# Kernel tuning notes

Hardware: AMD Instinct MI355X
Metric: run time of the kernel (lower is better)

## Reference

```python
import jax, jax.numpy as jnp
import numpy as np

NUM_BFS_ROUNDS = 32      # fixed-iteration replacement for the set-based BFS (enough hops for N=4096, k=20)
VORONOI_CHUNK = 1024     # must divide B*N


def _knn_self(points, K):
    # brute-force self-KNN over [B,N,3]; idx[...,0] is the query point itself
    sq = jnp.sum(points * points, -1)
    dist = sq[:, :, None] + sq[:, None, :] - 2.0 * jnp.einsum('bnd,bmd->bnm', points, points)
    N = points.shape[1]
    dist = jnp.where(jnp.eye(N, dtype=bool)[None], -1.0, dist)  # force self to rank first
    _, idx = jax.lax.top_k(-dist, K)
    return idx  # [B,N,K] int32


def _gather(x, idx):
    # x [B,N,D], idx [B,N,K] -> [B,N,K,D]
    return jax.vmap(lambda xb, ib: xb[ib])(x, idx)


def _disambiguate(normals, idx):
    # BFS normal-orientation propagation from point 0 (frontier shared across batch, as in the torch code)
    B, N, _ = normals.shape
    frontier0 = jnp.zeros((N,), bool).at[0].set(True)
    visited0 = jnp.zeros((N,), bool)

    def step(carry, _):
        nrm, visited, frontier = carry
        safe_idx = jnp.where(frontier[None, :, None], idx, N)  # non-frontier rows scatter to dummy slot N
        cur = _gather(nrm, idx)                                 # [B,N,K,3]
        sign = jnp.where(jnp.sum(cur * cur[:, :, 0:1, :], -1, keepdims=True) > 0, 1.0, -1.0)
        renew = cur * sign

        def scat(nb, ib, rb):
            pad = jnp.concatenate([nb, jnp.zeros((1, 3), nb.dtype)], 0)
            return pad.at[ib.reshape(-1)].set(rb.reshape(-1, 3))[:N]

        nrm = jax.vmap(scat)(nrm, safe_idx, renew)
        mark = jnp.zeros((N + 1,), bool).at[safe_idx[:, :, 1:].reshape(-1)].set(True)[:N]
        visited = visited | frontier
        frontier = mark & ~visited
        return (nrm, visited, frontier), None

    (normals, _, _), _ = jax.lax.scan(step, (normals, visited0, frontier0), None, length=NUM_BFS_ROUNDS)
    return normals


def _frames_field(points, idx):
    knn_pts = _gather(points, idx)                              # [B,N,K,3]
    centered = knn_pts - knn_pts.mean(-2, keepdims=True)
    # NOTE: divides by (last_dim - 1) == 2, faithfully replicating the original code
    cov = jnp.einsum('bnki,bnkj->bnij', centered, centered) / 2.0
    _, vecs = jnp.linalg.eigh(cov)                              # ascending eigenvalues
    frames = jnp.swapaxes(vecs, -1, -2)                         # rows = eigenvectors; row 0 = normal
    frames = frames.at[:, :, 0, :].set(_disambiguate(frames[:, :, 0, :], idx))
    det = jnp.linalg.det(frames)
    frames = frames.at[:, :, 1, :].set(frames[:, :, 1, :] * det[..., None])
    return frames, knn_pts


def _forward(points, k, local_W):
    B, N = points.shape[:2]
    idx = _knn_self(points, k)
    frames, knn_pts = _frames_field(points, idx)
    dpt = knn_pts - points[:, :, None, :]                       # [B,N,K,3]
    t1 = frames[:, :, 1, :]
    t2 = frames[:, :, 2, :]
    dpt_t = jnp.stack([jnp.sum(dpt * t1[:, :, None, :], -1),
                       jnp.sum(dpt * t2[:, :, None, :], -1)], -1)   # [B,N,K,2]

    # ---- local voronoi area on tangent-plane grid ----
    bmin = dpt_t.min(-2) * 1.1                                  # [B,N,2]
    bmax = dpt_t.max(-2) * 1.1
    maxlen = (bmax - bmin).max(-1)                              # [B,N]
    coord = (dpt_t - bmin[:, :, None, :]) / maxlen[:, :, None, None] * 2.0 - 1.0
    lin = jnp.linspace(-1.0, 1.0, local_W, dtype=points.dtype)
    X, Y = jnp.meshgrid(lin, lin, indexing='ij')
    grid = jnp.stack([X, Y], -1).reshape(-1, 2)                 # [W^2, 2]
    coords_c = jax.lax.stop_gradient(coord).reshape(-1, VORONOI_CHUNK, k, 2)

    def chunk_count(c):  # c [C,k,2] -> count of grid cells whose nearest local point is the center (idx 0)
        d = jnp.sum((grid[None, :, None, :] - c[:, None, :, :]) ** 2, -1)  # [C,W^2,k]
        return jnp.sum(jnp.argmin(d, -1) == 0, -1)

    counts = jax.lax.map(chunk_count, coords_c).reshape(B, N).astype(points.dtype)
    area = counts * maxlen ** 2 / float((local_W - 1) ** 2)     # [B,N]

    # ---- Weingarten fields (non-strict branch) -> gaussian curvature ----
    normals = frames[:, :, 0, :]
    dnrm = _gather(normals, idx) - normals[:, :, None, :]
    dnrm_t = jnp.stack([jnp.sum(dnrm * t1[:, :, None, :], -1),
                        jnp.sum(dnrm * t2[:, :, None, :], -1)], -1)  # [B,N,K,2]
    XXT = jnp.einsum('bnki,bnkj->bnij', dpt_t, dpt_t)
    YXT = jnp.einsum('bnki,bnkj->bnij', dnrm_t, dpt_t)
    Wmat = YXT @ jnp.linalg.inv(XXT + 1e-8 * jnp.eye(2, dtype=points.dtype))
    Wmat = (Wmat + jnp.swapaxes(Wmat, -1, -2)) / 2.0
    gauss = jnp.linalg.det(Wmat)                                # [B,N]

    euler = jnp.sum(gauss * area, -1) / np.pi / 2.0             # [B]
    return euler


def setup_inputs() -> dict:
    key = jax.random.key(0)
    pointscloud = jax.random.normal(key, (2, 4096, 3), dtype=jnp.float32)
    return {"pointscloud": pointscloud, "k": 20, "local_W": 64}


def reference(pointscloud, k, local_W):
    return _forward(pointscloud, k, local_W)
```

## Files before the change

### kernel.cpp

```cpp
#include <hip/hip_runtime.h>
#include <math.h>

#define NPTS  4096
#define BATCH 2
#define KNB   20
#define WGRID 64
#define GCELLS (WGRID * WGRID)
#define NROUNDS 32
#define KBUF  192
#define KQ    16
#define NEDGE (BATCH * NPTS * KNB)
#define NPACK (NEDGE / 16)

__global__ __launch_bounds__(256) void prep_kernel(const float* __restrict__ pts,
                                                   float4* __restrict__ pts4) {
    const int i = blockIdx.x * 256 + threadIdx.x;
    const float x = pts[i * 3 + 0], y = pts[i * 3 + 1], z = pts[i * 3 + 2];
    pts4[i] = make_float4(x, y, z, x * x + y * y + z * z);
}

__device__ __forceinline__ float knn_dist(const float4 c, const float px,
                                          const float py, const float pz,
                                          const float sqn, const int m,
                                          const int n) {
    const float dot = px * c.x + py * c.y + pz * c.z;
    float dist = (sqn + c.w) - 2.0f * dot;
    if (m == n) dist = -1.0f;
    return dist;
}

__device__ __forceinline__ unsigned long long knn_key(const float dist, const int m) {
    unsigned u = __float_as_uint(dist);
    u = (dist < 0.0f) ? ~u : (u | 0x80000000u);
    return ((unsigned long long)u << 32) | (unsigned)m;
}

__global__ __launch_bounds__(1024, 8) void knn_kernel(const float4* __restrict__ pts4,
                                                      int* __restrict__ idx) {
    const int tid  = threadIdx.x;
    const int lane = tid & 63;
    const int wid  = tid >> 6;
    const int q    = blockIdx.x * KQ + wid;
    const int b    = q >> 12;
    const int n    = q & (NPTS - 1);
    const float4* P4 = pts4 + (size_t)b * NPTS;

    __shared__ float4 spts[NPTS];
    __shared__ unsigned short buf[KQ][KBUF];

    for (int i = tid; i < NPTS; i += 1024) spts[i] = P4[i];
    __syncthreads();

    const float4 me = spts[n];
    const float px = me.x, py = me.y, pz = me.z, sqn = me.w;

    float lmin = 3e38f;
#pragma unroll
    for (int step = 0; step < 64; ++step) {
        const int m = lane + step * 64;
        lmin = fminf(lmin, knn_dist(spts[m], px, py, pz, sqn, m, n));
    }

    float v = lmin;
#pragma unroll
    for (int k = 2; k <= 64; k <<= 1) {
#pragma unroll
        for (int j = k >> 1; j >= 1; j >>= 1) {
            const float o = __shfl_xor(v, j, 64);
            const bool up    = ((lane & k) == 0);
            const bool lower = ((lane & j) == 0);
            v = (lower == up) ? fminf(v, o) : fmaxf(v, o);
        }
    }
    float thr = __shfl(v, 19, 64);
    thr = thr + fabsf(thr) * 1e-4f + 1e-6f;

    unsigned short* wbuf = buf[wid];
    int cnt = 0;
#pragma unroll
    for (int step = 0; step < 64; ++step) {
        const int m = lane + step * 64;
        const float dist = knn_dist(spts[m], px, py, pz, sqn, m, n);
        const bool keep = (dist <= thr);
        const unsigned long long mask = __ballot(keep);
        if (keep) {
            const int pos = cnt + __popcll(mask & ((1ull << lane) - 1ull));
            if (pos < KBUF) wbuf[pos] = (unsigned short)m;
        }
        cnt += __popcll(mask);
    }

    const int M = (cnt < KBUF) ? cnt : KBUF;
    int* op = idx + (size_t)q * KNB;
    const unsigned long long MAXK = ~0ull;
    if (M <= 64) {
        unsigned long long key = MAXK;
        if (lane < M) {
            const int m = (int)wbuf[lane];
            key = knn_key(knn_dist(spts[m], px, py, pz, sqn, m, n), m);
        }
#pragma unroll
        for (int k = 2; k <= 64; k <<= 1) {
#pragma unroll
            for (int j = k >> 1; j >= 1; j >>= 1) {
                const unsigned long long o = __shfl_xor(key, j, 64);
                const bool up    = ((lane & k) == 0);
                const bool lower = ((lane & j) == 0);
                const bool takeMin = (lower == up);
                const unsigned long long mn = key < o ? key : o;
                const unsigned long long mx = key < o ? o : key;
                key = takeMin ? mn : mx;
            }
        }
        if (lane < KNB) op[lane] = (int)(unsigned)(key & 0xffffffffu);
    } else {
        unsigned long long s0 = MAXK, s1 = MAXK, s2 = MAXK;
        if (lane < M) {
            const int m = (int)wbuf[lane];
            s0 = knn_key(knn_dist(spts[m], px, py, pz, sqn, m, n), m);
        }
        if (lane + 64 < M) {
            const int m = (int)wbuf[lane + 64];
            s1 = knn_key(knn_dist(spts[m], px, py, pz, sqn, m, n), m);
        }
        if (lane + 128 < M) {
            const int m = (int)wbuf[lane + 128];
            s2 = knn_key(knn_dist(spts[m], px, py, pz, sqn, m, n), m);
        }
#pragma unroll 1
        for (int r = 0; r < KNB; ++r) {
            unsigned long long kk = s0 < s1 ? s0 : s1;
            kk = kk < s2 ? kk : s2;
#pragma unroll
            for (int off = 32; off; off >>= 1) {
                const unsigned long long ok = __shfl_xor(kk, off, 64);
                kk = ok < kk ? ok : kk;
            }
            if (s0 == kk) s0 = MAXK;
            else if (s1 == kk) s1 = MAXK;
            else if (s2 == kk) s2 = MAXK;
            if (lane == 0) op[r] = (int)(unsigned)(kk & 0xffffffffu);
        }
    }
}

template <int p, int q, int r>
__device__ __forceinline__ void jrot(double A[3][3], double V[3][3]) {
    double apq = A[p][q];
    if (fabs(apq) < 1e-300) return;
    double app = A[p][p], aqq = A[q][q];
    double tau = (aqq - app) / (2.0 * apq);
    double sq  = sqrt(1.0 + tau * tau);
    double t   = (tau >= 0.0) ? (1.0 / (tau + sq)) : (1.0 / (tau - sq));
    double c   = 1.0 / sqrt(1.0 + t * t);
    double s   = t * c;
    A[p][p] = app - t * apq; A[q][q] = aqq + t * apq;
    A[p][q] = 0.0; A[q][p] = 0.0;
    double arp = A[r][p], arq = A[r][q];
    A[r][p] = c * arp - s * arq; A[p][r] = A[r][p];
    A[r][q] = s * arp + c * arq; A[q][r] = A[r][q];
#pragma unroll
    for (int i = 0; i < 3; ++i) {
        double vip = V[i][p], viq = V[i][q];
        V[i][p] = c * vip - s * viq;
        V[i][q] = s * vip + c * viq;
    }
}

__device__ __forceinline__ double selV(const double V[3][3], int i, int c) {
    return c == 0 ? V[i][0] : (c == 1 ? V[i][1] : V[i][2]);
}

__global__ __launch_bounds__(64) void frames_kernel(const float* __restrict__ pts,
                                                    const int* __restrict__ idx,
                                                    float* __restrict__ frames,
                                                    float* __restrict__ normals) {
    const int g = blockIdx.x * 64 + threadIdx.x;
    const int b = g / NPTS;
    const float* P  = pts + (size_t)b * NPTS * 3;
    const int*   ip = idx + (size_t)g * KNB;

    float mx = 0.f, my = 0.f, mz = 0.f;
#pragma unroll
    for (int k = 0; k < KNB; ++k) {
        const int j = ip[k];
        mx += P[j * 3 + 0]; my += P[j * 3 + 1]; mz += P[j * 3 + 2];
    }
    mx /= 20.0f; my /= 20.0f; mz /= 20.0f;

    float c00 = 0.f, c01 = 0.f, c02 = 0.f, c11 = 0.f, c12 = 0.f, c22 = 0.f;
#pragma unroll
    for (int k = 0; k < KNB; ++k) {
        const int j = ip[k];
        const float x = P[j * 3 + 0] - mx;
        const float y = P[j * 3 + 1] - my;
        const float z = P[j * 3 + 2] - mz;
        c00 += x * x; c01 += x * y; c02 += x * z;
        c11 += y * y; c12 += y * z; c22 += z * z;
    }
    c00 *= 0.5f; c01 *= 0.5f; c02 *= 0.5f; c11 *= 0.5f; c12 *= 0.5f; c22 *= 0.5f;

    double A[3][3] = {{c00, c01, c02}, {c01, c11, c12}, {c02, c12, c22}};
    double V[3][3] = {{1, 0, 0}, {0, 1, 0}, {0, 0, 1}};
#pragma unroll
    for (int sw = 0; sw < 10; ++sw) {
        jrot<0, 1, 2>(A, V);
        jrot<0, 2, 1>(A, V);
        jrot<1, 2, 0>(A, V);
    }
    double e0 = A[0][0], e1 = A[1][1], e2 = A[2][2];
    int o0 = 0, o1 = 1, o2 = 2;
    if (e0 > e1) { double t = e0; e0 = e1; e1 = t; int o = o0; o0 = o1; o1 = o; }
    if (e1 > e2) { double t = e1; e1 = e2; e2 = t; int o = o1; o1 = o2; o2 = o; }
    if (e0 > e1) { double t = e0; e0 = e1; e1 = t; int o = o0; o0 = o1; o1 = o; }

    float* F = frames + (size_t)g * 9;
    F[0] = (float)selV(V, 0, o0); F[1] = (float)selV(V, 1, o0); F[2] = (float)selV(V, 2, o0);
    F[3] = (float)selV(V, 0, o1); F[4] = (float)selV(V, 1, o1); F[5] = (float)selV(V, 2, o1);
    F[6] = (float)selV(V, 0, o2); F[7] = (float)selV(V, 1, o2); F[8] = (float)selV(V, 2, o2);
    normals[(size_t)g * 3 + 0] = F[0];
    normals[(size_t)g * 3 + 1] = F[1];
    normals[(size_t)g * 3 + 2] = F[2];
}

__global__ __launch_bounds__(256) void edgesign_kernel(const int* __restrict__ idx,
                                                       const float* __restrict__ normals,
                                                       unsigned* __restrict__ dsgnp,
                                                       unsigned short* __restrict__ idx16) {
    const int e = blockIdx.x * 256 + threadIdx.x;
    const int lane = threadIdx.x & 63;
    const int b = e / (NPTS * KNB);
    const int r = e - b * NPTS * KNB;
    const int n = r / KNB;
    const int j = idx[e];
    idx16[e] = (unsigned short)j;
    const float* NB = normals + (size_t)b * NPTS * 3;
    const float d = __fadd_rn(__fadd_rn(__fmul_rn(NB[j * 3 + 0], NB[n * 3 + 0]),
                                        __fmul_rn(NB[j * 3 + 1], NB[n * 3 + 1])),
                              __fmul_rn(NB[j * 3 + 2], NB[n * 3 + 2]));
    const unsigned long long m0 = __ballot(d == 0.0f);
    const unsigned long long m1 = __ballot(d > 0.0f);
    if (lane < 4) {
        unsigned x = (unsigned)(m0 >> (lane * 16)) & 0xFFFFu;
        unsigned y = (unsigned)(m1 >> (lane * 16)) & 0xFFFFu;
        x = (x | (x << 8)) & 0x00FF00FFu; x = (x | (x << 4)) & 0x0F0F0F0Fu;
        x = (x | (x << 2)) & 0x33333333u; x = (x | (x << 1)) & 0x55555555u;
        y = (y | (y << 8)) & 0x00FF00FFu; y = (y | (y << 4)) & 0x0F0F0F0Fu;
        y = (y | (y << 2)) & 0x33333333u; y = (y | (y << 1)) & 0x55555555u;
        dsgnp[((e - lane) >> 4) + lane] = x | (y << 1);
    }
}

__global__ __launch_bounds__(1024) void bfs_kernel(const unsigned short* __restrict__ idx16,
                                                   const unsigned* __restrict__ dsgnp,
                                                   float* __restrict__ nrm) {
    const int tid = threadIdx.x;
    const int lane = tid & 63;
    __shared__ int winner[BATCH * NPTS];
    __shared__ signed char sgbuf[2][BATCH * NPTS];
    __shared__ unsigned dsp[NPACK];
    __shared__ unsigned short list[NPTS];
    __shared__ unsigned char EL[NPTS];
    __shared__ int cntsh;

    for (int j = tid; j < NPTS; j += 1024) {
        winner[j] = 0; winner[NPTS + j] = 0;
        sgbuf[0][j] = 1; sgbuf[0][NPTS + j] = 1;
        EL[j] = 0;
    }
    for (int i = tid; i < NPACK; i += 1024) dsp[i] = dsgnp[i];
    if (tid == 0) { cntsh = 1; list[0] = 0; EL[0] = 1; }
    __syncthreads();

    int cur = 0;
    int rstart = 0, rend = 1;
    for (int round = 0; round < NROUNDS; ++round) {
        const int tag = (round + 1) << 17;
        const int items = (rend - rstart) * BATCH;
        for (int base = 0; base < items; base += 4096) {
            unsigned pr[4][KNB / 2];
            int tflat[4], wbase[4];
            bool ok[4];
#pragma unroll
            for (int s = 0; s < 4; ++s) {
                const int w = base + s * 1024 + tid;
                ok[s] = (w < items);
                if (ok[s]) {
                    const int i = w >> 1, b = w & 1;
                    const int n0 = (int)list[rstart + i];
                    tflat[s] = tag + n0 * KNB;
                    wbase[s] = b * NPTS;
                    const unsigned* rp =
                        (const unsigned*)(idx16 + ((size_t)b * NPTS + n0) * KNB);
#pragma unroll
                    for (int u = 0; u < KNB / 2; ++u) pr[s][u] = rp[u];
                }
            }
#pragma unroll
            for (int s = 0; s < 4; ++s) {
                if (ok[s]) {
#pragma unroll
                    for (int u = 0; u < KNB / 2; ++u) {
                        const int j0 = (int)(pr[s][u] & 0xffffu);
                        const int j1 = (int)(pr[s][u] >> 16);
                        atomicMax(&winner[wbase[s] + j0], tflat[s] + 2 * u);
                        atomicMax(&winner[wbase[s] + j1], tflat[s] + 2 * u + 1);
                    }
                }
            }
        }
        __syncthreads();
        const signed char* sgOld = sgbuf[cur];
        signed char* sgNew = sgbuf[cur ^ 1];
#pragma unroll
        for (int u = 0; u < 4; ++u) {
            const int j = tid + u * 1024;
            bool marked = false;
#pragma unroll
            for (int b = 0; b < BATCH; ++b) {
                const int bj = b * NPTS + j;
                const int w = winner[bj];
                signed char s = sgOld[bj];
                if (w >= tag) {
                    const int flat = w - tag;
                    const int nsrc = flat / KNB;
                    const int wi = b * (NPTS * KNB) + flat;
                    const int d = (int)((dsp[wi >> 4] >> ((wi & 15) << 1)) & 3u) - 1;
                    const signed char sn = sgOld[b * NPTS + nsrc];
                    s = d ? (signed char)(d * sn) : (signed char)(-s);
                    if (flat % KNB != 0) marked = true;
                }
                sgNew[bj] = s;
            }
            const bool f = marked && !EL[j];
            if (f) EL[j] = 1;
            const unsigned long long mask = __ballot(f);
            if (mask) {
                const int lead = (int)(__ffsll((long long)mask) - 1);
                int basep = 0;
                if (lane == lead) basep = atomicAdd(&cntsh, (int)__popcll(mask));
                basep = __shfl(basep, lead, 64);
                if (f) list[basep + (int)__popcll(mask & ((1ull << lane) - 1ull))] =
                           (unsigned short)j;
            }
        }
        __syncthreads();
        cur ^= 1;
        rstart = rend;
        rend = cntsh;
        if (rstart == rend) break;
    }
    const signed char* sgF = sgbuf[cur];
    for (int i = tid; i < BATCH * NPTS * 3; i += 1024) {
        if (sgF[i / 3] < 0) nrm[i] = -nrm[i];
    }
}

__global__ __launch_bounds__(256) void geom_kernel(const float* __restrict__ pts,
                                                   const int* __restrict__ idx,
                                                   const float* __restrict__ frames,
                                                   const float* __restrict__ nrm,
                                                   double* __restrict__ pervals) {
    const int lane = threadIdx.x & 63;
    const int q = blockIdx.x * 4 + (threadIdx.x >> 6);
    const int b = q >> 12, n = q & (NPTS - 1);
    const float* P  = pts + (size_t)b * NPTS * 3;
    const float* NR = nrm + (size_t)b * NPTS * 3;
    const float* F  = frames + (size_t)q * 9;

    const float v0x = NR[n * 3 + 0], v0y = NR[n * 3 + 1], v0z = NR[n * 3 + 2];
    const float v1x = F[3], v1y = F[4], v1z = F[5];
    const float v2x = F[6], v2y = F[7], v2z = F[8];
    const float det = v0x * (v1y * v2z - v1z * v2y)
                    - v0y * (v1x * v2z - v1z * v2x)
                    + v0z * (v1x * v2y - v1y * v2x);
    const float t1x = v1x * det, t1y = v1y * det, t1z = v1z * det;
    const float t2x = v2x, t2y = v2y, t2z = v2z;

    const bool isk = lane < KNB;
    float ptx = 0.f, pty = 0.f, qtx = 0.f, qty = 0.f;
    if (isk) {
        const int j = idx[(size_t)q * KNB + lane];
        const float dx = P[j * 3 + 0] - P[n * 3 + 0];
        const float dy = P[j * 3 + 1] - P[n * 3 + 1];
        const float dz = P[j * 3 + 2] - P[n * 3 + 2];
        ptx = dx * t1x + dy * t1y + dz * t1z;
        pty = dx * t2x + dy * t2y + dz * t2z;
        const float ex = NR[j * 3 + 0] - v0x;
        const float ey = NR[j * 3 + 1] - v0y;
        const float ez = NR[j * 3 + 2] - v0z;
        qtx = ex * t1x + ey * t1y + ez * t1z;
        qty = ex * t2x + ey * t2y + ez * t2z;
    }

    float mnx = isk ? ptx :  3e38f, mny = isk ? pty :  3e38f;
    float mxx = isk ? ptx : -3e38f, mxy = isk ? pty : -3e38f;
#pragma unroll
    for (int off = 32; off; off >>= 1) {
        mnx = fminf(mnx, __shfl_xor(mnx, off, 64));
        mny = fminf(mny, __shfl_xor(mny, off, 64));
        mxx = fmaxf(mxx, __shfl_xor(mxx, off, 64));
        mxy = fmaxf(mxy, __shfl_xor(mxy, off, 64));
    }
    mnx *= 1.1f; mny *= 1.1f; mxx *= 1.1f; mxy *= 1.1f;
    const float ml = fmaxf(mxx - mnx, mxy - mny);

    const float cx = (ptx - mnx) / ml * 2.0f - 1.0f;
    const float cy = (pty - mny) / ml * 2.0f - 1.0f;
    const float c0x = __shfl(cx, 0, 64), c0y = __shfl(cy, 0, 64);

    const float ax = 2.0f * (cx - c0x);
    const float ay = 2.0f * (cy - c0y);
    const float bbk = cx * cx + cy * cy - (c0x * c0x + c0y * c0y);
    const float inva = (ay != 0.0f) ? (1.0f / ay) : 0.0f;

    const float gx = (float)(-1.0 + (2.0 * (double)lane) / 63.0);
    float lo = -3e38f, hi = 3e38f;
    bool feas = true;
#pragma unroll
    for (int k = 1; k < KNB; ++k) {
        const float axk = __shfl(ax, k, 64);
        const float ayk = __shfl(ay, k, 64);
        const float bk  = __shfl(bbk, k, 64);
        const float ik  = __shfl(inva, k, 64);
        const float rk  = bk - gx * axk;
        const float t   = rk * ik;
        if (ayk > 0.0f)      hi = fminf(hi, t);
        else if (ayk < 0.0f) lo = fmaxf(lo, t);
        else                 feas = feas && (rk >= 0.0f);
    }
    int cnt = 0;
    if (feas) {
        const float hif = fminf((hi + 1.0f) * 31.5f, 63.0f);
        const float lof = fmaxf((lo + 1.0f) * 31.5f, 0.0f);
        const int jhi = (int)floorf(hif);
        const int jlo = (int)ceilf(lof);
        cnt = jhi - jlo + 1;
        if (cnt < 0) cnt = 0;
    }
#pragma unroll
    for (int off = 32; off; off >>= 1) cnt += __shfl_xor(cnt, off, 64);
    const float area = (float)cnt * ml * ml / 3969.0f;

    double xx00 = 0, xx01 = 0, xx11 = 0, yx00 = 0, yx01 = 0, yx10 = 0, yx11 = 0;
    if (isk) {
        const double px = ptx, py = pty, qx2 = qtx, qy2 = qty;
        xx00 = px * px; xx01 = px * py; xx11 = py * py;
        yx00 = qx2 * px; yx01 = qx2 * py; yx10 = qy2 * px; yx11 = qy2 * py;
    }
#pragma unroll
    for (int off = 32; off; off >>= 1) {
        xx00 += __shfl_xor(xx00, off, 64);
        xx01 += __shfl_xor(xx01, off, 64);
        xx11 += __shfl_xor(xx11, off, 64);
        yx00 += __shfl_xor(yx00, off, 64);
        yx01 += __shfl_xor(yx01, off, 64);
        yx10 += __shfl_xor(yx10, off, 64);
        yx11 += __shfl_xor(yx11, off, 64);
    }
    if (lane == 0) {
        const double m00 = xx00 + 1e-8, m01 = xx01, m11 = xx11 + 1e-8;
        const double dm = m00 * m11 - m01 * m01;
        const double i00 = m11 / dm, i01 = -m01 / dm, i11 = m00 / dm;
        const double w00 = yx00 * i00 + yx01 * i01;
        const double w01 = yx00 * i01 + yx01 * i11;
        const double w10 = yx10 * i00 + yx11 * i01;
        const double w11 = yx10 * i01 + yx11 * i11;
        const double off2 = 0.5 * (w01 + w10);
        const double gauss = w00 * w11 - off2 * off2;
        pervals[q] = gauss * (double)area;
    }
}

__global__ __launch_bounds__(256) void reduce_kernel(const double* __restrict__ pervals,
                                                     float* __restrict__ out) {
    const int b = blockIdx.x, tid = threadIdx.x;
    __shared__ double sm[256];
    double s = 0.0;
    for (int i = tid; i < NPTS; i += 256) s += pervals[(size_t)b * NPTS + i];
    sm[tid] = s;
    __syncthreads();
    for (int st = 128; st > 0; st >>= 1) {
        if (tid < st) sm[tid] += sm[tid + st];
        __syncthreads();
    }
    if (tid == 0) out[b] = (float)(sm[0] / 3.14159265358979323846 / 2.0);
}

extern "C" void kernel_launch(void* const* d_in, const int* in_sizes, int n_in,
                              void* d_out, int out_size, void* d_ws, size_t ws_size,
                              hipStream_t stream) {
    (void)in_sizes; (void)n_in; (void)out_size; (void)ws_size;
    const float* pts = (const float*)d_in[0];
    char* ws = (char*)d_ws;

    size_t off = 0;
    double* pervals = (double*)(ws + off); off += (size_t)BATCH * NPTS * sizeof(double);
    int*    idx     = (int*)(ws + off);    off += (size_t)BATCH * NPTS * KNB * sizeof(int);
    float*  frames  = (float*)(ws + off);  off += (size_t)BATCH * NPTS * 9 * sizeof(float);
    float*  normals = (float*)(ws + off);  off += (size_t)BATCH * NPTS * 3 * sizeof(float);
    unsigned short* idx16 = (unsigned short*)(ws + off);
    off += (size_t)BATCH * NPTS * KNB * sizeof(unsigned short);
    unsigned* dsgnp = (unsigned*)(ws + off);
    off += (size_t)NPACK * sizeof(unsigned);
    off = (off + 15) & ~(size_t)15;
    float4* pts4 = (float4*)(ws + off);

    prep_kernel<<<BATCH * NPTS / 256, 256, 0, stream>>>(pts, pts4);
    knn_kernel<<<BATCH * NPTS / KQ, 1024, 0, stream>>>(pts4, idx);
    frames_kernel<<<BATCH * NPTS / 64, 64, 0, stream>>>(pts, idx, frames, normals);
    edgesign_kernel<<<BATCH * NPTS * KNB / 256, 256, 0, stream>>>(idx, normals, dsgnp, idx16);
    bfs_kernel<<<1, 1024, 0, stream>>>(idx16, dsgnp, normals);
    geom_kernel<<<BATCH * NPTS / 4, 256, 0, stream>>>(pts, idx, frames, normals, pervals);
    reduce_kernel<<<BATCH, 256, 0, stream>>>(pervals, (float*)d_out);
}
```

Before: 105.3 us.

## Encode sign outcome into BFS atomicMax winner value and vectorize resolve pass

The BFS kernel now computes each candidate's resulting sign and its 'marked' flag at scatter time and packs them into the low bits of the atomicMax value, together with the flat edge index and the round tag. The resolve pass no longer needs a shared-memory copy of the packed sign table or a divide to recover the source node. It reads winner and sign data four at a time with vector loads, and compacts the new frontier with a wave prefix sum. This removes the initial shared-memory load of dsgnp and the division and lookup work in the resolve step. In exchange, each scatter does extra global loads and bit arithmetic, and the tag shift grows to leave room for the packed fields.

```diff
diff --git a/kernel.cpp b/kernel.cpp
--- a/kernel.cpp
+++ b/kernel.cpp
@@ -258,7 +258,6 @@
     const int lane = tid & 63;
     __shared__ int winner[BATCH * NPTS];
     __shared__ signed char sgbuf[2][BATCH * NPTS];
-    __shared__ unsigned dsp[NPACK];
     __shared__ unsigned short list[NPTS];
     __shared__ unsigned char EL[NPTS];
     __shared__ int cntsh;
@@ -268,81 +267,116 @@
         sgbuf[0][j] = 1; sgbuf[0][NPTS + j] = 1;
         EL[j] = 0;
     }
-    for (int i = tid; i < NPACK; i += 1024) dsp[i] = dsgnp[i];
     if (tid == 0) { cntsh = 1; list[0] = 0; EL[0] = 1; }
     __syncthreads();
 
     int cur = 0;
     int rstart = 0, rend = 1;
     for (int round = 0; round < NROUNDS; ++round) {
-        const int tag = (round + 1) << 17;
+        const int tag = (round + 1) << 20;
+        const signed char* sgOld = sgbuf[cur];
+        signed char* sgNew = sgbuf[cur ^ 1];
+
         const int items = (rend - rstart) * BATCH;
         for (int base = 0; base < items; base += 4096) {
             unsigned pr[4][KNB / 2];
-            int tflat[4], wbase[4];
+            unsigned long long dd[4];
+            int vbase[4], wbase[4], sn_[4];
             bool ok[4];
 #pragma unroll
-            for (int s = 0; s < 4; ++s) {
-                const int w = base + s * 1024 + tid;
-                ok[s] = (w < items);
-                if (ok[s]) {
+            for (int s4 = 0; s4 < 4; ++s4) {
+                const int w = base + s4 * 1024 + tid;
+                ok[s4] = (w < items);
+                if (ok[s4]) {
                     const int i = w >> 1, b = w & 1;
                     const int n0 = (int)list[rstart + i];
-                    tflat[s] = tag + n0 * KNB;
-                    wbase[s] = b * NPTS;
+                    const int flatb = n0 * KNB;
+                    vbase[s4] = tag | (flatb << 3);
+                    wbase[s4] = b * NPTS;
+                    sn_[s4] = (int)sgOld[b * NPTS + n0];
                     const unsigned* rp =
                         (const unsigned*)(idx16 + ((size_t)b * NPTS + n0) * KNB);
 #pragma unroll
-                    for (int u = 0; u < KNB / 2; ++u) pr[s][u] = rp[u];
+                    for (int u = 0; u < KNB / 2; ++u) pr[s4][u] = rp[u];
+                    const int wi = b * (NPTS * KNB) + flatb;
+                    const unsigned w0 = dsgnp[wi >> 4];
+                    const unsigned w1 = dsgnp[(wi >> 4) + 1];
+                    dd[s4] = ((unsigned long long)w0 |
+                              ((unsigned long long)w1 << 32)) >> ((wi & 15) * 2);
                 }
             }
 #pragma unroll
-            for (int s = 0; s < 4; ++s) {
-                if (ok[s]) {
+            for (int s4 = 0; s4 < 4; ++s4) {
+                if (ok[s4]) {
+                    const unsigned long long d = dd[s4];
+                    const int sn = sn_[s4];
 #pragma unroll
                     for (int u = 0; u < KNB / 2; ++u) {
-                        const int j0 = (int)(pr[s][u] & 0xffffu);
-                        const int j1 = (int)(pr[s][u] >> 16);
-                        atomicMax(&winner[wbase[s] + j0], tflat[s] + 2 * u);
-                        atomicMax(&winner[wbase[s] + j1], tflat[s] + 2 * u + 1);
+                        const int j0 = (int)(pr[s4][u] & 0xffffu);
+                        const int j1 = (int)(pr[s4][u] >> 16);
+                        const int k0 = 2 * u, k1 = 2 * u + 1;
+                        const int c0 = (int)((d >> (2 * k0)) & 3u);
+                        const int c1 = (int)((d >> (2 * k1)) & 3u);
+                        int op0 = (c0 == 1) ? 0 : (2 | ((((c0 - 1) * sn) > 0) ? 1 : 0));
+                        int op1 = (c1 == 1) ? 0 : (2 | ((((c1 - 1) * sn) > 0) ? 1 : 0));
+                        const int m0 = (k0 != 0) ? 4 : 0;
+                        atomicMax(&winner[wbase[s4] + j0],
+                                  vbase[s4] | (k0 << 3) | m0 | op0);
+                        atomicMax(&winner[wbase[s4] + j1],
+                                  vbase[s4] | (k1 << 3) | 4 | op1);
                     }
                 }
             }
         }
         __syncthreads();
-        const signed char* sgOld = sgbuf[cur];
-        signed char* sgNew = sgbuf[cur ^ 1];
-#pragma unroll
-        for (int u = 0; u < 4; ++u) {
-            const int j = tid + u * 1024;
-            bool marked = false;
-#pragma unroll
-            for (int b = 0; b < BATCH; ++b) {
-                const int bj = b * NPTS + j;
-                const int w = winner[bj];
-                signed char s = sgOld[bj];
+
+        int fmask = 0;
+#pragma unroll
+        for (int b = 0; b < BATCH; ++b) {
+            const int jb = b * NPTS + tid * 4;
+            const int4 w4 = *(const int4*)&winner[jb];
+            const unsigned sg4 = *(const unsigned*)&sgOld[jb];
+            unsigned ns4 = 0;
+            const int wv0 = w4.x, wv1 = w4.y, wv2 = w4.z, wv3 = w4.w;
+#pragma unroll
+            for (int t = 0; t < 4; ++t) {
+                const int w = (t == 0) ? wv0 : (t == 1) ? wv1 : (t == 2) ? wv2 : wv3;
+                int s = (int)(signed char)(sg4 >> (8 * t));
                 if (w >= tag) {
-                    const int flat = w - tag;
-                    const int nsrc = flat / KNB;
-                    const int wi = b * (NPTS * KNB) + flat;
-                    const int d = (int)((dsp[wi >> 4] >> ((wi & 15) << 1)) & 3u) - 1;
-                    const signed char sn = sgOld[b * NPTS + nsrc];
-                    s = d ? (signed char)(d * sn) : (signed char)(-s);
-                    if (flat % KNB != 0) marked = true;
+                    s = (w & 2) ? ((w & 1) ? 1 : -1) : -s;
+                    fmask |= ((w >> 2) & 1) << t;
                 }
-                sgNew[bj] = s;
-            }
-            const bool f = marked && !EL[j];
-            if (f) EL[j] = 1;
-            const unsigned long long mask = __ballot(f);
-            if (mask) {
-                const int lead = (int)(__ffsll((long long)mask) - 1);
-                int basep = 0;
-                if (lane == lead) basep = atomicAdd(&cntsh, (int)__popcll(mask));
-                basep = __shfl(basep, lead, 64);
-                if (f) list[basep + (int)__popcll(mask & ((1ull << lane) - 1ull))] =
-                           (unsigned short)j;
-            }
+                ns4 |= ((unsigned)(unsigned char)(signed char)s) << (8 * t);
+            }
+            *(unsigned*)&sgNew[jb] = ns4;
+        }
+
+        int c = 0, addmask = 0;
+        if (fmask) {
+#pragma unroll
+            for (int t = 0; t < 4; ++t) {
+                const int j = tid * 4 + t;
+                if (((fmask >> t) & 1) && !EL[j]) {
+                    EL[j] = 1; addmask |= 1 << t; ++c;
+                }
+            }
+        }
+        const unsigned long long any = __ballot(c != 0);
+        if (any) {
+            int pre = c;
+#pragma unroll
+            for (int i = 1; i < 64; i <<= 1) {
+                const int t = __shfl_up(pre, i, 64);
+                if (lane >= i) pre += t;
+            }
+            const int total = __shfl(pre, 63, 64);
+            int bb = 0;
+            if (lane == 63) bb = atomicAdd(&cntsh, total);
+            bb = __shfl(bb, 63, 64);
+            int off = bb + pre - c;
+#pragma unroll
+            for (int t = 0; t < 4; ++t)
+                if ((addmask >> t) & 1) list[off++] = (unsigned short)(tid * 4 + t);
         }
         __syncthreads();
         cur ^= 1;
```

After: 109.2 us. +3.7%, slower.

## Make BFS update sparse over touched nodes with per-edge parallel scatter

Applied to the files above, without the earlier changes.

The BFS kernel's per-round update no longer sweeps all 2x4096 nodes. It records the nodes first reached by the atomicMax scatter in a compacted touched list and updates signs only for those. The scatter phase is also re-parallelised so each thread handles one edge rather than one frontier node's 20 neighbours, and double-buffered sign arrays are replaced by a single array plus a snapshot of frontier signs. This adds extra ballot/atomic compaction work, an atomicExch on an int-widened EL array, and more LDS use.

```diff
diff --git a/kernel.cpp b/kernel.cpp
--- a/kernel.cpp
+++ b/kernel.cpp
@@ -257,102 +257,107 @@
     const int tid = threadIdx.x;
     const int lane = tid & 63;
     __shared__ int winner[BATCH * NPTS];
-    __shared__ signed char sgbuf[2][BATCH * NPTS];
+    __shared__ signed char sg[BATCH * NPTS];
+    __shared__ signed char fsg[BATCH * NPTS];
     __shared__ unsigned dsp[NPACK];
     __shared__ unsigned short list[NPTS];
-    __shared__ unsigned char EL[NPTS];
+    __shared__ int EL[NPTS];
+    __shared__ unsigned short touched[BATCH * NPTS];
     __shared__ int cntsh;
+    __shared__ int tc[2];
 
     for (int j = tid; j < NPTS; j += 1024) {
         winner[j] = 0; winner[NPTS + j] = 0;
-        sgbuf[0][j] = 1; sgbuf[0][NPTS + j] = 1;
+        sg[j] = 1; sg[NPTS + j] = 1;
         EL[j] = 0;
     }
     for (int i = tid; i < NPACK; i += 1024) dsp[i] = dsgnp[i];
-    if (tid == 0) { cntsh = 1; list[0] = 0; EL[0] = 1; }
+    if (tid == 0) { cntsh = 1; list[0] = 0; EL[0] = 1; tc[0] = 0; tc[1] = 0; }
     __syncthreads();
 
-    int cur = 0;
     int rstart = 0, rend = 1;
     for (int round = 0; round < NROUNDS; ++round) {
         const int tag = (round + 1) << 17;
+        const int par = round & 1;
         const int items = (rend - rstart) * BATCH;
-        for (int base = 0; base < items; base += 4096) {
-            unsigned pr[4][KNB / 2];
-            int tflat[4], wbase[4];
-            bool ok[4];
-#pragma unroll
-            for (int s = 0; s < 4; ++s) {
-                const int w = base + s * 1024 + tid;
-                ok[s] = (w < items);
-                if (ok[s]) {
-                    const int i = w >> 1, b = w & 1;
-                    const int n0 = (int)list[rstart + i];
-                    tflat[s] = tag + n0 * KNB;
-                    wbase[s] = b * NPTS;
-                    const unsigned* rp =
-                        (const unsigned*)(idx16 + ((size_t)b * NPTS + n0) * KNB);
-#pragma unroll
-                    for (int u = 0; u < KNB / 2; ++u) pr[s][u] = rp[u];
+
+        for (int w = tid; w < items; w += 1024) {
+            const int i = w >> 1, b = w & 1;
+            const int n0 = (int)list[rstart + i];
+            fsg[b * NPTS + n0] = sg[b * NPTS + n0];
+        }
+
+        const int edges = items * KNB;
+        for (int base = 0; base < edges; base += 1024) {
+            const int e = base + tid;
+            bool first = false;
+            int tj = 0, tb = 0;
+            if (e < edges) {
+                const int item = e / KNB;
+                const int k = e - item * KNB;
+                const int i = item >> 1;
+                tb = item & 1;
+                const int n0 = (int)list[rstart + i];
+                const int j = (int)idx16[((size_t)tb * NPTS + n0) * KNB + k];
+                const int old = atomicMax(&winner[tb * NPTS + j],
+                                          tag + n0 * KNB + k);
+                first = (old < tag);
+                tj = j;
+            }
+            const unsigned long long mask = __ballot(first);
+            if (mask) {
+                const int lead = (int)(__ffsll((long long)mask) - 1);
+                int basep = 0;
+                if (lane == lead) basep = atomicAdd(&tc[par], (int)__popcll(mask));
+                basep = __shfl(basep, lead, 64);
+                if (first)
+                    touched[basep + (int)__popcll(mask & ((1ull << lane) - 1ull))] =
+                        (unsigned short)((tb << 12) | tj);
+            }
+        }
+        __syncthreads();
+        const int nt = tc[par];
+        if (tid == 0) tc[par ^ 1] = 0;
+
+        for (int base = 0; base < nt; base += 1024) {
+            const int w = base + tid;
+            bool f = false;
+            int tj = 0;
+            if (w < nt) {
+                const unsigned t = touched[w];
+                const int b = (int)(t >> 12);
+                tj = (int)(t & 4095);
+                const int bj = b * NPTS + tj;
+                const int flat = winner[bj] - tag;
+                const int nsrc = flat / KNB;
+                const int wi = b * (NPTS * KNB) + flat;
+                const int d = (int)((dsp[wi >> 4] >> ((wi & 15) << 1)) & 3u) - 1;
+                const signed char sn = fsg[b * NPTS + nsrc];
+                const signed char s =
+                    d ? (signed char)(d * sn) : (signed char)(-sg[bj]);
+                sg[bj] = s;
+                if (flat - nsrc * KNB != 0) {
+                    if (atomicExch(&EL[tj], 1) == 0) f = true;
                 }
             }
-#pragma unroll
-            for (int s = 0; s < 4; ++s) {
-                if (ok[s]) {
-#pragma unroll
-                    for (int u = 0; u < KNB / 2; ++u) {
-                        const int j0 = (int)(pr[s][u] & 0xffffu);
-                        const int j1 = (int)(pr[s][u] >> 16);
-                        atomicMax(&winner[wbase[s] + j0], tflat[s] + 2 * u);
-                        atomicMax(&winner[wbase[s] + j1], tflat[s] + 2 * u + 1);
-                    }
-                }
-            }
-        }
-        __syncthreads();
-        const signed char* sgOld = sgbuf[cur];
-        signed char* sgNew = sgbuf[cur ^ 1];
-#pragma unroll
-        for (int u = 0; u < 4; ++u) {
-            const int j = tid + u * 1024;
-            bool marked = false;
-#pragma unroll
-            for (int b = 0; b < BATCH; ++b) {
-                const int bj = b * NPTS + j;
-                const int w = winner[bj];
-                signed char s = sgOld[bj];
-                if (w >= tag) {
-                    const int flat = w - tag;
-                    const int nsrc = flat / KNB;
-                    const int wi = b * (NPTS * KNB) + flat;
-                    const int d = (int)((dsp[wi >> 4] >> ((wi & 15) << 1)) & 3u) - 1;
-                    const signed char sn = sgOld[b * NPTS + nsrc];
-                    s = d ? (signed char)(d * sn) : (signed char)(-s);
-                    if (flat % KNB != 0) marked = true;
-                }
-                sgNew[bj] = s;
-            }
-            const bool f = marked && !EL[j];
-            if (f) EL[j] = 1;
             const unsigned long long mask = __ballot(f);
             if (mask) {
                 const int lead = (int)(__ffsll((long long)mask) - 1);
                 int basep = 0;
                 if (lane == lead) basep = atomicAdd(&cntsh, (int)__popcll(mask));
                 basep = __shfl(basep, lead, 64);
-                if (f) list[basep + (int)__popcll(mask & ((1ull << lane) - 1ull))] =
-                           (unsigned short)j;
+                if (f)
+                    list[basep + (int)__popcll(mask & ((1ull << lane) - 1ull))] =
+                        (unsigned short)tj;
             }
         }
         __syncthreads();
-        cur ^= 1;
         rstart = rend;
         rend = cntsh;
         if (rstart == rend) break;
     }
-    const signed char* sgF = sgbuf[cur];
     for (int i = tid; i < BATCH * NPTS * 3; i += 1024) {
-        if (sgF[i / 3] < 0) nrm[i] = -nrm[i];
+        if (sg[i / 3] < 0) nrm[i] = -nrm[i];
     }
 }
 
```

Measured after the change: 157.2 us. 1.49x slower.
